# Kernel tuning notes

Hardware: AMD Instinct MI355X
Metric: run time of the kernel (lower is better)

## Reference

```python
import jax, jax.numpy as jnp
import numpy as np

KSIZE = 3
KN = (KSIZE - 1) // 2  # 1
TEMP = 50.0


def _extract_patches(x, same_pad):
    """TF tf.image.extract_patches ordering: per location, (dy, dx, channel).
    x: [b,H,W,d] -> [b,h,w,9*d] (h=H,w=W if same_pad else H-2,W-2)."""
    if same_pad:
        x = jnp.pad(x, ((0, 0), (KN, KN), (KN, KN), (0, 0)))
    b, Hp, Wp, d = x.shape
    h, w = Hp - 2 * KN, Wp - 2 * KN
    slices = [x[:, dy:dy + h, dx:dx + w, :]
              for dy in range(KSIZE) for dx in range(KSIZE)]
    return jnp.concatenate(slices, axis=-1)


def setup_inputs() -> dict:
    key = jax.random.key(0)
    k1, k2, k3 = jax.random.split(key, 3)
    b, h, w, dims = 4, 48, 48, 64
    g_in = jax.random.normal(k1, (b, h, w, dims), dtype=jnp.float32)
    # binary inpainting mask (1 = known background, 0 = hole)
    mask = (jax.random.uniform(k2, (b, h, w, 1)) > 0.5).astype(jnp.float32)
    W2 = jax.random.normal(k3, (2 * dims, dims), dtype=jnp.float32) / np.sqrt(2.0 * dims)
    b2 = jnp.zeros((dims,), dtype=jnp.float32)
    return {"g_in": g_in, "mask": mask, "W2": W2, "b2": b2}


def reference(g_in, mask, W2, b2):
    b, h, w, dims = g_in.shape
    c = (h - 2 * KN) * (w - 2 * KN)

    mask_r = mask  # already (h,w,1); broadcasts over dims (== tile)
    bg = g_in * mask_r

    # p1: VALID 3x3 patches of bg -> dynamic kernels, [b, c, 9*dims]
    p1 = _extract_patches(bg, same_pad=False).reshape(b, c, KSIZE * KSIZE * dims)
    # p2: SAME 3x3 patches of g_in, [b, h, w, 9*dims]
    p2 = _extract_patches(g_in, same_pad=True)

    # cross-correlation: conv2d(ft, k1) == per-location dot with each bg patch
    CS = jnp.einsum('byxk,bjk->byxj', p2, p1)              # [b,h,w,c]
    k1d = jnp.sum(p1 * p1, axis=2)                          # [b,c]
    wwd = jnp.sum(p2 * p2, axis=3, keepdims=True)           # [b,h,w,1]
    DS1 = k1d[:, None, None, :] + wwd - 2.0 * CS            # squared distances
    mu = jnp.mean(DS1, axis=3, keepdims=True)
    sd = jnp.std(DS1, axis=3, keepdims=True)                # population std (tf.math.reduce_std)
    DS2 = -jnp.tanh((DS1 - mu) / sd)
    CA = jax.nn.softmax(TEMP * DS2, axis=-1)                # [b,h,w,c]

    # transposed conv aggregation with per-sample kernels k2[b,j,dy,dx,ch]
    k2 = p1.reshape(b, c, KSIZE, KSIZE, dims)
    CA_pad = jnp.pad(CA, ((0, 0), (KN, KN), (KN, KN), (0, 0)))
    acl = jnp.zeros((b, h, w, dims), dtype=g_in.dtype)
    for dy in range(KSIZE):
        for dx in range(KSIZE):
            win = CA_pad[:, 2 * KN - dy:2 * KN - dy + h, 2 * KN - dx:2 * KN - dx + w, :]
            acl = acl + jnp.einsum('byxj,bjd->byxd', win, k2[:, :, dy, dx, :])
    acl = acl / 9.0

    ACL = bg + acl * (1.0 - mask_r)
    con1 = jnp.concatenate([g_in, ACL], axis=3)             # [b,h,w,2*dims]
    return jax.nn.elu(jnp.einsum('byxk,kd->byxd', con1, W2) + b2)
```

## Files before the change

kernel.cpp:

```cpp
#include <hip/hip_runtime.h>
#include <hip/hip_fp16.h>
#include <math.h>

#define BB 4
#define HH 48
#define WW 48
#define DD 64
#define CH 46
#define CWp 46
#define CC (CH*CWp)
#define KK 576
#define HWp (HH*WW)
#define KPAD 2176
#define KSPLIT0 1088
#define PW 50
#define PP (PW*PW)

typedef __attribute__((ext_vector_type(8))) short short8;
typedef __attribute__((ext_vector_type(4))) float float4v;

#define OFFB_GPAD  ((size_t)0)
#define OFFB_BGPAD ((size_t)1280000)
#define OFFB_E     ((size_t)2560000)
#define OFFB_K1D   ((size_t)2596864)
#define OFFB_P1T   ((size_t)2630720)
#define OFFB_S     ((size_t)12657728)
#define OFFB_AGG0  ((size_t)52765760)
#define OFFB_AGG1  ((size_t)63382592)

__device__ __forceinline__ ushort f2bf(float x) {
    unsigned u = __float_as_uint(x);
    return (ushort)((u + 0x7FFFu + ((u >> 16) & 1u)) >> 16);
}

__device__ __forceinline__ float waveReduceSum(float x) {
#pragma unroll
    for (int o = 32; o > 0; o >>= 1) x += __shfl_down(x, o, 64);
    return x;
}

__device__ __forceinline__ float blockReduceSum(float x, float* sm) {
#pragma unroll
    for (int o = 32; o > 0; o >>= 1) x += __shfl_down(x, o, 64);
    int lane = threadIdx.x & 63, w = threadIdx.x >> 6;
    __syncthreads();
    if (lane == 0) sm[w] = x;
    __syncthreads();
    return sm[0] + sm[1] + sm[2] + sm[3];
}

__device__ __forceinline__ float fast_tanh(float z) {
    float e = __expf(2.f * z);
    return 1.f - 2.f / (e + 1.f);
}

typedef __attribute__((address_space(3))) void lds_void_t;
typedef __attribute__((address_space(1))) void gmem_void_t;
__device__ __forceinline__ void gld16(const ushort* g, ushort* lds) {
    __builtin_amdgcn_global_load_lds((gmem_void_t*)g, (lds_void_t*)lds, 16, 0, 0);
}

__global__ __launch_bounds__(256) void build_pads(const float* __restrict__ g,
                                                  const float* __restrict__ mask,
                                                  ushort* __restrict__ gpad,
                                                  ushort* __restrict__ bgpad,
                                                  float* __restrict__ e) {
    int w = threadIdx.x >> 6, c = threadIdx.x & 63;
    int q4 = blockIdx.x * 4 + w;
    int b = q4 / PP, q = q4 % PP;
    int yp = q / PW, xp = q % PW;
    size_t o = (size_t)q4 * DD + c;
    if (yp >= 1 && yp <= HH && xp >= 1 && xp <= WW) {
        int pix = (yp - 1) * WW + (xp - 1);
        float gv = g[((size_t)b * HWp + pix) * DD + c];
        float m  = mask[(size_t)b * HWp + pix];
        float bgv = gv * m;
        gpad[o]  = f2bf(gv);
        bgpad[o] = f2bf(bgv);
        float ss = waveReduceSum(bgv * bgv);
        if (c == 0) e[b * HWp + pix] = ss;
    } else {
        gpad[o] = 0;
        bgpad[o] = 0;
    }
}

__global__ __launch_bounds__(256) void build_p1t(const ushort* __restrict__ bgpad,
                                                 const float* __restrict__ e,
                                                 ushort* __restrict__ p1t,
                                                 float* __restrict__ k1d) {
    int d9 = blockIdx.y, b = blockIdx.z;
    int t = threadIdx.x;
    if (blockIdx.x == 34) {
        int jg = (b * 9 + d9) * 256 + t;
        if (jg < BB * CC) {
            int bb = jg / CC, j = jg % CC;
            int jy = j / CWp, jx = j - jy * CWp;
            const float* eb = e + bb * HWp + jy * WW + jx;
            float s = 0.f;
#pragma unroll
            for (int ddy = 0; ddy < 3; ddy++)
#pragma unroll
                for (int ddx = 0; ddx < 3; ddx++) s += eb[ddy * WW + ddx];
            k1d[jg] = s;
        }
        return;
    }
    __shared__ ushort T[64 * 65];
    int jt = blockIdx.x;
    int dy = d9 / 3, dx = d9 - dy * 3;
    const ushort* src = bgpad + (size_t)b * PP * DD;
    int lr = t >> 3, c8 = (t & 7) * 8;
#pragma unroll
    for (int pass = 0; pass < 2; pass++) {
        int r = lr + pass * 32;
        int j = jt * 64 + r;
        uint4 d = make_uint4(0, 0, 0, 0);
        if (j < CC) {
            int jy = j / CWp, jx = j - jy * CWp;
            d = *(const uint4*)(src + (size_t)((jy + dy + 1) * PW + (jx + dx + 1)) * DD + c8);
        }
        ushort tmp[8];
        *(uint4*)tmp = d;
#pragma unroll
        for (int u = 0; u < 8; u++) T[r * 65 + c8 + u] = tmp[u];
    }
    __syncthreads();
#pragma unroll
    for (int pass = 0; pass < 2; pass++) {
        int c = lr + pass * 32;
        int j8 = (t & 7) * 8;
        ushort tmp[8];
#pragma unroll
        for (int u = 0; u < 8; u++) tmp[u] = T[(j8 + u) * 65 + c];
        *(uint4*)(p1t + ((size_t)b * KK + d9 * 64 + c) * KPAD + jt * 64 + j8) = *(const uint4*)tmp;
    }
}

__global__ __launch_bounds__(256) void gemm1_nt(const ushort* __restrict__ gpad,
                                                const ushort* __restrict__ bgpad,
                                                __half* __restrict__ Cout) {
    __shared__ ushort As[2 * 4096];
    __shared__ ushort Bs[2 * 4096];
    int i0 = blockIdx.x;
    int b = (i0 & 7) >> 1;
    int tile = ((i0 >> 3) << 1) | (i0 & 1);
    int ty = tile / 17, tx = tile - ty * 17;
    int m0 = ty * 128, n0 = tx * 128;
    const ushort* Ag = gpad + (size_t)b * PP * DD;
    const ushort* Bg = bgpad + (size_t)b * PP * DD;

    int tid = threadIdx.x;
    int l = tid & 63, w = tid >> 6;
    int quad = l >> 4, l15 = l & 15;
    int sw8 = (l15 >> 1) & 3;
    int wm = (w >> 1) * 64, wn = (w & 1) * 64;
    int rowInC = l >> 2;
    int cSw = (l & 3) ^ ((l >> 3) & 3);

    int baseA[2], baseB[2];
    bool vB[2];
#pragma unroll
    for (int i = 0; i < 2; i++) {
        int rg = w * 2 + i;
        int r = rg * 16 + rowInC;
        int p = m0 + r;
        int y = p / WW, x = p - y * WW;
        baseA[i] = (y * PW + x) * DD + cSw * 8;
        int n = n0 + r;
        vB[i] = (n < CC);
        int jy = 0, jx = 0;
        if (vB[i]) { jy = n / CWp; jx = n - jy * CWp; }
        baseB[i] = ((jy + 1) * PW + (jx + 1)) * DD + cSw * 8;
    }

    float4v acc[4][4];
#pragma unroll
    for (int i = 0; i < 4; i++)
#pragma unroll
        for (int j = 0; j < 4; j++) acc[i][j] = (float4v){0.f, 0.f, 0.f, 0.f};

#pragma unroll
    for (int i = 0; i < 2; i++) {
        int rg = w * 2 + i;
        gld16(Ag + baseA[i], As + rg * 512);
        if (vB[i]) gld16(Bg + baseB[i], Bs + rg * 512);
    }

    int buf = 0;
    for (int k0 = 0; k0 < KK; k0 += 32) {
        __syncthreads();
        int nb = buf ^ 1;
        int kn = k0 + 32;
        if (kn < KK) {
            int d9 = kn >> 6;
            int dy = d9 / 3, dx = d9 - dy * 3;
            int off = (dy * PW + dx) * DD + (kn & 63);
#pragma unroll
            for (int i = 0; i < 2; i++) {
                int rg = w * 2 + i;
                gld16(Ag + baseA[i] + off, As + nb * 4096 + rg * 512);
                if (vB[i]) gld16(Bg + baseB[i] + off, Bs + nb * 4096 + rg * 512);
            }
        }
        const ushort* Ax = As + buf * 4096;
        const ushort* Bx = Bs + buf * 4096;
        short8 af[4], bf[4];
#pragma unroll
        for (int i = 0; i < 4; i++)
            af[i] = *(const short8*)&Ax[(wm + i * 16 + l15) * 32 + ((quad ^ sw8)) * 8];
#pragma unroll
        for (int j = 0; j < 4; j++)
            bf[j] = *(const short8*)&Bx[(wn + j * 16 + l15) * 32 + ((quad ^ sw8)) * 8];
#pragma unroll
        for (int i = 0; i < 4; i++)
#pragma unroll
            for (int j = 0; j < 4; j++)
                acc[i][j] = __builtin_amdgcn_mfma_f32_16x16x32_bf16(af[i], bf[j], acc[i][j], 0, 0, 0);
        buf = nb;
    }

    __half* C = Cout + (size_t)b * HWp * KPAD;
#pragma unroll
    for (int i = 0; i < 4; i++) {
#pragma unroll
        for (int j = 0; j < 4; j++) {
            int n = n0 + wn + j * 16 + l15;
            if (n < CC) {
#pragma unroll
                for (int r = 0; r < 4; r++) {
                    int m = m0 + wm + i * 16 + quad * 4 + r;
                    C[(size_t)m * KPAD + n] = __float2half(acc[i][j][r]);
                }
            }
        }
    }
}

template <int NF, bool NMASK>
__device__ __forceinline__ void gemm_tile_db(const ushort* __restrict__ Ab,
                                             const ushort* __restrict__ Bb,
                                             int lda, int ldb, int kb, int ke,
                                             int Nrem,
                                             ushort* As, ushort* Bs,
                                             float4v (&acc)[4][NF]) {
    constexpr int NBI = NF / 2;
    constexpr int BBUF = 2048 * NBI;
    int tid = threadIdx.x;
    int l = tid & 63, w = tid >> 6;
    int quad = l >> 4, l15 = l & 15;
    int sw8 = (l15 >> 1) & 3;
    int wm = (w >> 1) * 64, wn = (w & 1) * (NF * 16);
    int rowInC = l >> 2;
    int cSw = (l & 3) ^ ((l >> 3) & 3);

#pragma unroll
    for (int i = 0; i < 2; i++) {
        int rg = w * 2 + i;
        gld16(Ab + (size_t)(rg * 16 + rowInC) * lda + kb + cSw * 8, As + rg * 512);
    }
#pragma unroll
    for (int i = 0; i < NBI; i++) {
        int rg = w * NBI + i;
        int r = rg * 16 + rowInC;
        if (!NMASK || r < Nrem)
            gld16(Bb + (size_t)r * ldb + kb + cSw * 8, Bs + rg * 512);
    }

    int buf = 0;
    for (int k0 = kb; k0 < ke; k0 += 32) {
        __syncthreads();
        int nb = buf ^ 1;
        if (k0 + 32 < ke) {
#pragma unroll
            for (int i = 0; i < 2; i++) {
                int rg = w * 2 + i;
                gld16(Ab + (size_t)(rg * 16 + rowInC) * lda + (k0 + 32) + cSw * 8,
                      As + nb * 4096 + rg * 512);
            }
#pragma unroll
            for (int i = 0; i < NBI; i++) {
                int rg = w * NBI + i;
                int r = rg * 16 + rowInC;
                if (!NMASK || r < Nrem)
                    gld16(Bb + (size_t)r * ldb + (k0 + 32) + cSw * 8,
                          Bs + nb * BBUF + rg * 512);
            }
        }
        const ushort* Ax = As + buf * 4096;
        const ushort* Bx = Bs + buf * BBUF;
        short8 af[4], bf[NF];
#pragma unroll
        for (int i = 0; i < 4; i++)
            af[i] = *(const short8*)&Ax[(wm + i * 16 + l15) * 32 + ((quad ^ sw8)) * 8];
#pragma unroll
        for (int j = 0; j < NF; j++)
            bf[j] = *(const short8*)&Bx[(wn + j * 16 + l15) * 32 + ((quad ^ sw8)) * 8];
#pragma unroll
        for (int i = 0; i < 4; i++)
#pragma unroll
            for (int j = 0; j < NF; j++)
                acc[i][j] = __builtin_amdgcn_mfma_f32_16x16x32_bf16(af[i], bf[j], acc[i][j], 0, 0, 0);
        buf = nb;
    }
}

__global__ __launch_bounds__(256) void gemm2_split(const ushort* __restrict__ A,
                                                   const ushort* __restrict__ Bt,
                                                   __half* __restrict__ agg0,
                                                   __half* __restrict__ agg1) {
    __shared__ ushort As[2 * 4096];
    __shared__ ushort Bs[2 * 6144];
    int i0 = blockIdx.x;
    int z = i0 & 7;
    int b = z >> 1, split = z & 1;
    int tile = i0 >> 3;
    int ty = tile / 3, tx = tile - ty * 3;
    int m0 = ty * 128, n0 = tx * 192;
    const ushort* Ab = A + (size_t)b * HWp * KPAD + (size_t)m0 * KPAD;
    const ushort* Bb = Bt + (size_t)b * KK * KPAD + (size_t)n0 * KPAD;
    float4v acc[4][6];
#pragma unroll
    for (int i = 0; i < 4; i++)
#pragma unroll
        for (int j = 0; j < 6; j++) acc[i][j] = (float4v){0.f, 0.f, 0.f, 0.f};

    gemm_tile_db<6, false>(Ab, Bb, KPAD, KPAD, split ? KSPLIT0 : 0,
                           split ? KPAD : KSPLIT0, 192, As, Bs, acc);

    int tid = threadIdx.x;
    int lane = tid & 63, wid = tid >> 6;
    int quad = lane >> 4, l15 = lane & 15;
    int wm = (wid >> 1) * 64, wn = (wid & 1) * 96;
    __half* C = (split ? agg1 : agg0) + (size_t)b * HWp * KK;
#pragma unroll
    for (int i = 0; i < 4; i++) {
#pragma unroll
        for (int j = 0; j < 6; j++) {
            int n = n0 + wn + j * 16 + l15;
#pragma unroll
            for (int r = 0; r < 4; r++) {
                int m = m0 + wm + i * 16 + quad * 4 + r;
                C[(size_t)m * KK + n] = __float2half(acc[i][j][r]);
            }
        }
    }
}

__global__ __launch_bounds__(256) void rowsoft(void* __restrict__ Sbase,
                                               const float* __restrict__ k1d) {
    __shared__ float sm[4];
    size_t row = blockIdx.x;
    int b = (int)(row / HWp);
    const __half* p = (const __half*)Sbase + row * KPAD;
    ushort* wout = (ushort*)Sbase + row * KPAD;
    const float* k1 = k1d + (size_t)b * CC;
    int t = threadIdx.x;
    bool hasx = t < 34;

    uint4 raw = *(const uint4*)(p + t * 8);
    uint rx = hasx ? *(const uint*)(p + 2048 + t * 2) : 0u;
    float v[8], vx[2];
    {
        const __half2* h2 = (const __half2*)&raw;
#pragma unroll
        for (int i = 0; i < 4; i++) {
            float2 f = __half22float2(h2[i]);
            v[2 * i] = f.x; v[2 * i + 1] = f.y;
        }
        __half2 hx = *(__half2*)&rx;
        float2 fx = __half22float2(hx);
        vx[0] = fx.x; vx[1] = fx.y;
    }
    {
        const float* kp = k1 + t * 8;
#pragma unroll
        for (int i = 0; i < 8; i++) v[i] = kp[i] - 2.f * v[i];
        if (hasx) {
            vx[0] = k1[2048 + t * 2] - 2.f * vx[0];
            vx[1] = k1[2048 + t * 2 + 1] - 2.f * vx[1];
        }
    }
    float s = 0.f;
#pragma unroll
    for (int i = 0; i < 8; i++) s += v[i];
    if (hasx) s += vx[0] + vx[1];
    s = blockReduceSum(s, sm);
    float mu = s / (float)CC;
    float vs = 0.f;
#pragma unroll
    for (int i = 0; i < 8; i++) { float d = v[i] - mu; vs += d * d; }
    if (hasx) { float d0 = vx[0] - mu, d1 = vx[1] - mu; vs += d0 * d0 + d1 * d1; }
    vs = blockReduceSum(vs, sm);
    float inv_sd = 1.f / sqrtf(vs / (float)CC);
    float es = 0.f;
#pragma unroll
    for (int i = 0; i < 8; i++) {
        v[i] = __expf(-50.f * fast_tanh((v[i] - mu) * inv_sd));
        es += v[i];
    }
    if (hasx) {
        vx[0] = __expf(-50.f * fast_tanh((vx[0] - mu) * inv_sd));
        vx[1] = __expf(-50.f * fast_tanh((vx[1] - mu) * inv_sd));
        es += vx[0] + vx[1];
    }
    es = blockReduceSum(es, sm);
    float invz = 1.f / es;

    ushort o[8];
#pragma unroll
    for (int i = 0; i < 8; i++) o[i] = f2bf(v[i] * invz);
    *(uint4*)(wout + t * 8) = *(const uint4*)o;
    if (hasx) {
        ushort ox[2] = { f2bf(vx[0] * invz), f2bf(vx[1] * invz) };
        *(uint*)(wout + 2048 + t * 2) = *(const uint*)ox;
    } else {
        *(uint*)(wout + CC + 2 * (t - 34)) = 0u;
    }
}

__global__ __launch_bounds__(256) void final_k(const float* __restrict__ g,
                                               const float* __restrict__ mask,
                                               const __half* __restrict__ agg0,
                                               const __half* __restrict__ agg1,
                                               const float* __restrict__ W2,
                                               const float* __restrict__ b2,
                                               float* __restrict__ out) {
    int w = threadIdx.x >> 6, d = threadIdx.x & 63;
    int pix = blockIdx.x * 4 + w;
    int b = pix / HWp, yx = pix % HWp;
    int y = yx / WW, x = yx % WW;

    __shared__ float con1[4][128];
    float acl = 0.f;
#pragma unroll
    for (int dy = 0; dy < 3; dy++) {
#pragma unroll
        for (int dx = 0; dx < 3; dx++) {
            int yy = y + 1 - dy, xx = x + 1 - dx;
            if (yy >= 0 && yy < HH && xx >= 0 && xx < WW) {
                size_t off = ((size_t)(b * HWp + yy * WW + xx)) * KK + (dy * 3 + dx) * DD + d;
                acl += __half2float(agg0[off]) + __half2float(agg1[off]);
            }
        }
    }
    float m = mask[pix];
    float gv = g[(size_t)pix * DD + d];
    float bgv = gv * m;
    float ACL = bgv + (acl / 9.f) * (1.f - m);
    con1[w][d] = gv;
    con1[w][64 + d] = ACL;
    __syncthreads();
    float accv = b2[d];
#pragma unroll 8
    for (int k = 0; k < 128; k++) accv = fmaf(con1[w][k], W2[k * 64 + d], accv);
    out[(size_t)pix * DD + d] = accv > 0.f ? accv : expm1f(accv);
}

extern "C" void kernel_launch(void* const* d_in, const int* in_sizes, int n_in,
                              void* d_out, int out_size, void* d_ws, size_t ws_size,
                              hipStream_t stream) {
    const float* g    = (const float*)d_in[0];
    const float* mask = (const float*)d_in[1];
    const float* W2   = (const float*)d_in[2];
    const float* b2   = (const float*)d_in[3];
    float* out = (float*)d_out;
    char* ws = (char*)d_ws;

    ushort* gpad  = (ushort*)(ws + OFFB_GPAD);
    ushort* bgpad = (ushort*)(ws + OFFB_BGPAD);
    float*  e     = (float*) (ws + OFFB_E);
    float*  k1d   = (float*) (ws + OFFB_K1D);
    ushort* p1t   = (ushort*)(ws + OFFB_P1T);
    void*   S     = (void*)  (ws + OFFB_S);
    __half* agg0  = (__half*)(ws + OFFB_AGG0);
    __half* agg1  = (__half*)(ws + OFFB_AGG1);

    build_pads<<<BB * PP / 4, 256, 0, stream>>>(g, mask, gpad, bgpad, e);
    build_p1t<<<dim3(35, 9, BB), 256, 0, stream>>>(bgpad, e, p1t, k1d);

    gemm1_nt<<<dim3(1224), 256, 0, stream>>>(gpad, bgpad, (__half*)S);

    rowsoft<<<BB * HWp, 256, 0, stream>>>(S, k1d);

    gemm2_split<<<dim3(432), 256, 0, stream>>>((const ushort*)S, p1t, agg0, agg1);

    final_k<<<BB * HWp / 4, 256, 0, stream>>>(g, mask, agg0, agg1, W2, b2, out);
}
```

Before: 187.9 us.

## Factor patch correlation into pixel-level Gram matrix plus 3x3 stencil sums

```diff
diff --git a/kernel.cpp b/kernel.cpp
--- a/kernel.cpp
+++ b/kernel.cpp
@@ -7,14 +7,15 @@
 #define WW 48
 #define DD 64
 #define CH 46
-#define CWp 46
-#define CC (CH*CWp)
-#define KK 576
+#define CC (CH*CH)
 #define HWp (HH*WW)
-#define KPAD 2176
-#define KSPLIT0 1088
 #define PW 50
 #define PP (PW*PW)
+#define UST 2512
+#define CAST 2120
+#define QN 2304
+#define NSPL 8
+#define KCH (QN/NSPL)
 
 typedef __attribute__((ext_vector_type(8))) short short8;
 typedef __attribute__((ext_vector_type(4))) float float4v;
@@ -23,14 +24,18 @@
 #define OFFB_BGPAD ((size_t)1280000)
 #define OFFB_E     ((size_t)2560000)
 #define OFFB_K1D   ((size_t)2596864)
-#define OFFB_P1T   ((size_t)2630720)
-#define OFFB_S     ((size_t)12657728)
-#define OFFB_AGG0  ((size_t)52765760)
-#define OFFB_AGG1  ((size_t)63382592)
+#define OFFB_BGT   ((size_t)2630720)
+#define OFFB_U     ((size_t)3810368)
+#define OFFB_CA    ((size_t)54050368)
+#define OFFB_WGT   ((size_t)93126208)
+#define OFFB_ACLP  ((size_t)135593536)
 
 __device__ __forceinline__ ushort f2bf(float x) {
     unsigned u = __float_as_uint(x);
     return (ushort)((u + 0x7FFFu + ((u >> 16) & 1u)) >> 16);
+}
+__device__ __forceinline__ float bf2f(ushort h) {
+    return __uint_as_float((unsigned)h << 16);
 }
 
 __device__ __forceinline__ float waveReduceSum(float x) {
@@ -85,94 +90,83 @@
     }
 }
 
-__global__ __launch_bounds__(256) void build_p1t(const ushort* __restrict__ bgpad,
-                                                 const float* __restrict__ e,
-                                                 ushort* __restrict__ p1t,
-                                                 float* __restrict__ k1d) {
-    int d9 = blockIdx.y, b = blockIdx.z;
+__global__ __launch_bounds__(256) void build_bgt_k1d(const ushort* __restrict__ bgpad,
+                                                     const float* __restrict__ e,
+                                                     ushort* __restrict__ bgT,
+                                                     float* __restrict__ k1d) {
     int t = threadIdx.x;
-    if (blockIdx.x == 34) {
-        int jg = (b * 9 + d9) * 256 + t;
+    if (blockIdx.x < 144) {
+        int b = blockIdx.x / 36, tile = blockIdx.x % 36;
+        __shared__ ushort T[64 * 65];
+        const ushort* src = bgpad + (size_t)b * PP * DD;
+        int lr = t >> 3, c8 = (t & 7) * 8;
+#pragma unroll
+        for (int pass = 0; pass < 2; pass++) {
+            int r = lr + pass * 32;
+            int p = tile * 64 + r;
+            int py = p / 48 + 1, px = p % 48 + 1;
+            uint4 d = *(const uint4*)(src + (size_t)(py * PW + px) * DD + c8);
+            ushort tmp[8];
+            *(uint4*)tmp = d;
+#pragma unroll
+            for (int u = 0; u < 8; u++) T[r * 65 + c8 + u] = tmp[u];
+        }
+        __syncthreads();
+        ushort* dst = bgT + (size_t)b * DD * QN;
+#pragma unroll
+        for (int pass = 0; pass < 2; pass++) {
+            int c = lr + pass * 32;
+            int j8 = (t & 7) * 8;
+            ushort tmp[8];
+#pragma unroll
+            for (int u = 0; u < 8; u++) tmp[u] = T[(j8 + u) * 65 + c];
+            *(uint4*)(dst + (size_t)c * QN + tile * 64 + j8) = *(const uint4*)tmp;
+        }
+    } else {
+        int jg = (blockIdx.x - 144) * 256 + t;
         if (jg < BB * CC) {
-            int bb = jg / CC, j = jg % CC;
-            int jy = j / CWp, jx = j - jy * CWp;
-            const float* eb = e + bb * HWp + jy * WW + jx;
+            int b = jg / CC, j = jg % CC;
+            int jy = j / CH, jx = j - jy * CH;
+            const float* eb = e + b * HWp + jy * WW + jx;
             float s = 0.f;
 #pragma unroll
-            for (int ddy = 0; ddy < 3; ddy++)
-#pragma unroll
-                for (int ddx = 0; ddx < 3; ddx++) s += eb[ddy * WW + ddx];
+            for (int dy = 0; dy < 3; dy++)
+#pragma unroll
+                for (int dx = 0; dx < 3; dx++) s += eb[dy * WW + dx];
             k1d[jg] = s;
         }
-        return;
-    }
-    __shared__ ushort T[64 * 65];
-    int jt = blockIdx.x;
-    int dy = d9 / 3, dx = d9 - dy * 3;
-    const ushort* src = bgpad + (size_t)b * PP * DD;
-    int lr = t >> 3, c8 = (t & 7) * 8;
-#pragma unroll
-    for (int pass = 0; pass < 2; pass++) {
-        int r = lr + pass * 32;
-        int j = jt * 64 + r;
-        uint4 d = make_uint4(0, 0, 0, 0);
-        if (j < CC) {
-            int jy = j / CWp, jx = j - jy * CWp;
-            d = *(const uint4*)(src + (size_t)((jy + dy + 1) * PW + (jx + dx + 1)) * DD + c8);
-        }
-        ushort tmp[8];
-        *(uint4*)tmp = d;
-#pragma unroll
-        for (int u = 0; u < 8; u++) T[r * 65 + c8 + u] = tmp[u];
-    }
-    __syncthreads();
-#pragma unroll
-    for (int pass = 0; pass < 2; pass++) {
-        int c = lr + pass * 32;
-        int j8 = (t & 7) * 8;
-        ushort tmp[8];
-#pragma unroll
-        for (int u = 0; u < 8; u++) tmp[u] = T[(j8 + u) * 65 + c];
-        *(uint4*)(p1t + ((size_t)b * KK + d9 * 64 + c) * KPAD + jt * 64 + j8) = *(const uint4*)tmp;
-    }
-}
-
-__global__ __launch_bounds__(256) void gemm1_nt(const ushort* __restrict__ gpad,
-                                                const ushort* __restrict__ bgpad,
-                                                __half* __restrict__ Cout) {
-    __shared__ ushort As[2 * 4096];
-    __shared__ ushort Bs[2 * 4096];
+    }
+}
+
+__global__ __launch_bounds__(256) void ugemm(const ushort* __restrict__ gpad,
+                                             const ushort* __restrict__ bgpad,
+                                             __half* __restrict__ U) {
+    __shared__ ushort As[128 * 64];
+    __shared__ ushort Bs[128 * 64];
     int i0 = blockIdx.x;
     int b = (i0 & 7) >> 1;
     int tile = ((i0 >> 3) << 1) | (i0 & 1);
-    int ty = tile / 17, tx = tile - ty * 17;
-    int m0 = ty * 128, n0 = tx * 128;
+    int ty = tile / 20, tx = tile - ty * 20;
+    int p0 = ty * 128, q0 = tx * 128;
     const ushort* Ag = gpad + (size_t)b * PP * DD;
     const ushort* Bg = bgpad + (size_t)b * PP * DD;
 
     int tid = threadIdx.x;
     int l = tid & 63, w = tid >> 6;
     int quad = l >> 4, l15 = l & 15;
-    int sw8 = (l15 >> 1) & 3;
+    int sw = l15 & 7;
     int wm = (w >> 1) * 64, wn = (w & 1) * 64;
-    int rowInC = l >> 2;
-    int cSw = (l & 3) ^ ((l >> 3) & 3);
-
-    int baseA[2], baseB[2];
-    bool vB[2];
-#pragma unroll
-    for (int i = 0; i < 2; i++) {
-        int rg = w * 2 + i;
-        int r = rg * 16 + rowInC;
-        int p = m0 + r;
-        int y = p / WW, x = p - y * WW;
-        baseA[i] = (y * PW + x) * DD + cSw * 8;
-        int n = n0 + r;
-        vB[i] = (n < CC);
-        int jy = 0, jx = 0;
-        if (vB[i]) { jy = n / CWp; jx = n - jy * CWp; }
-        baseB[i] = ((jy + 1) * PW + (jx + 1)) * DD + cSw * 8;
-    }
+    int sr = l >> 3;
+    int gch = (l & 7) ^ (sr & 7);
+
+#pragma unroll
+    for (int i = 0; i < 4; i++) {
+        int rg = 4 * w + i;
+        int r = rg * 8 + sr;
+        if (p0 + r < PP) gld16(Ag + (size_t)(p0 + r) * DD + gch * 8, As + rg * 512);
+        if (q0 + r < PP) gld16(Bg + (size_t)(q0 + r) * DD + gch * 8, Bs + rg * 512);
+    }
+    __syncthreads();
 
     float4v acc[4][4];
 #pragma unroll
@@ -181,59 +175,137 @@
         for (int j = 0; j < 4; j++) acc[i][j] = (float4v){0.f, 0.f, 0.f, 0.f};
 
 #pragma unroll
-    for (int i = 0; i < 2; i++) {
-        int rg = w * 2 + i;
-        gld16(Ag + baseA[i], As + rg * 512);
-        if (vB[i]) gld16(Bg + baseB[i], Bs + rg * 512);
-    }
-
-    int buf = 0;
-    for (int k0 = 0; k0 < KK; k0 += 32) {
-        __syncthreads();
-        int nb = buf ^ 1;
-        int kn = k0 + 32;
-        if (kn < KK) {
-            int d9 = kn >> 6;
-            int dy = d9 / 3, dx = d9 - dy * 3;
-            int off = (dy * PW + dx) * DD + (kn & 63);
-#pragma unroll
-            for (int i = 0; i < 2; i++) {
-                int rg = w * 2 + i;
-                gld16(Ag + baseA[i] + off, As + nb * 4096 + rg * 512);
-                if (vB[i]) gld16(Bg + baseB[i] + off, Bs + nb * 4096 + rg * 512);
-            }
-        }
-        const ushort* Ax = As + buf * 4096;
-        const ushort* Bx = Bs + buf * 4096;
+    for (int h = 0; h < 2; h++) {
         short8 af[4], bf[4];
 #pragma unroll
         for (int i = 0; i < 4; i++)
-            af[i] = *(const short8*)&Ax[(wm + i * 16 + l15) * 32 + ((quad ^ sw8)) * 8];
+            af[i] = *(const short8*)&As[(wm + i * 16 + l15) * 64 + ((h * 4 + quad) ^ sw) * 8];
 #pragma unroll
         for (int j = 0; j < 4; j++)
-            bf[j] = *(const short8*)&Bx[(wn + j * 16 + l15) * 32 + ((quad ^ sw8)) * 8];
+            bf[j] = *(const short8*)&Bs[(wn + j * 16 + l15) * 64 + ((h * 4 + quad) ^ sw) * 8];
 #pragma unroll
         for (int i = 0; i < 4; i++)
 #pragma unroll
             for (int j = 0; j < 4; j++)
                 acc[i][j] = __builtin_amdgcn_mfma_f32_16x16x32_bf16(af[i], bf[j], acc[i][j], 0, 0, 0);
-        buf = nb;
-    }
-
-    __half* C = Cout + (size_t)b * HWp * KPAD;
+    }
+
+    __half* Ub = U + (size_t)b * PP * UST;
 #pragma unroll
     for (int i = 0; i < 4; i++) {
 #pragma unroll
         for (int j = 0; j < 4; j++) {
-            int n = n0 + wn + j * 16 + l15;
-            if (n < CC) {
+            int n = q0 + wn + j * 16 + l15;
+            if (n < PP) {
 #pragma unroll
                 for (int r = 0; r < 4; r++) {
-                    int m = m0 + wm + i * 16 + quad * 4 + r;
-                    C[(size_t)m * KPAD + n] = __float2half(acc[i][j][r]);
+                    int m = p0 + wm + i * 16 + quad * 4 + r;
+                    if (m < PP) Ub[(size_t)m * UST + n] = __float2half(acc[i][j][r]);
                 }
             }
         }
+    }
+}
+
+__global__ __launch_bounds__(256) void cs_softmax(const __half* __restrict__ U,
+                                                  const float* __restrict__ k1d,
+                                                  ushort* __restrict__ CA) {
+    __shared__ float sm[4];
+    int i0 = blockIdx.x;
+    int b = (i0 & 7) >> 1;
+    int m = ((i0 >> 3) << 1) | (i0 & 1);
+    int y = m / 48, x = m - y * 48;
+    const __half* Ub = U + (size_t)b * PP * UST;
+    const float* k1 = k1d + b * CC;
+    const __half* rows[9];
+#pragma unroll
+    for (int dy = 0; dy < 3; dy++)
+#pragma unroll
+        for (int dx = 0; dx < 3; dx++)
+            rows[dy * 3 + dx] = Ub + (size_t)((y + dy) * PW + (x + dx)) * UST;
+
+    int t = threadIdx.x;
+    float v[9];
+#pragma unroll
+    for (int i = 0; i < 9; i++) {
+        int j = t + i * 256;
+        if (j < CC) {
+            int jy = j / CH, jx = j - jy * CH;
+            int base = (jy + 1) * PW + (jx + 1);
+            float cs = 0.f;
+#pragma unroll
+            for (int s = 0; s < 9; s++) {
+                int off = (s / 3) * PW + (s % 3);
+                cs += __half2float(rows[s][base + off]);
+            }
+            v[i] = k1[j] - 2.f * cs;
+        } else v[i] = 0.f;
+    }
+    float s0 = 0.f;
+#pragma unroll
+    for (int i = 0; i < 9; i++) { int j = t + i * 256; if (j < CC) s0 += v[i]; }
+    s0 = blockReduceSum(s0, sm);
+    float mu = s0 / (float)CC;
+    float vs = 0.f;
+#pragma unroll
+    for (int i = 0; i < 9; i++) {
+        int j = t + i * 256;
+        if (j < CC) { float d = v[i] - mu; vs += d * d; }
+    }
+    vs = blockReduceSum(vs, sm);
+    float inv_sd = 1.f / sqrtf(vs / (float)CC);
+    float es = 0.f;
+#pragma unroll
+    for (int i = 0; i < 9; i++) {
+        int j = t + i * 256;
+        if (j < CC) {
+            v[i] = __expf(-50.f * fast_tanh((v[i] - mu) * inv_sd));
+            es += v[i];
+        }
+    }
+    es = blockReduceSum(es, sm);
+    float invz = 1.f / es;
+    ushort* wout = CA + (size_t)(b * HWp + m) * CAST;
+#pragma unroll
+    for (int i = 0; i < 9; i++) {
+        int j = t + i * 256;
+        if (j < CAST) wout[j] = (j < CC) ? f2bf(v[i] * invz) : (ushort)0;
+    }
+}
+
+__global__ __launch_bounds__(256) void wgt_gather(const ushort* __restrict__ CA,
+                                                  ushort* __restrict__ Wgt) {
+    int i0 = blockIdx.x;
+    int b = (i0 & 7) >> 1;
+    int m = ((i0 >> 3) << 1) | (i0 & 1);
+    int y = m / 48, x = m - y * 48;
+    const ushort* CAb = CA + (size_t)b * HWp * CAST;
+    const ushort* rows[9];
+    bool val[9];
+#pragma unroll
+    for (int dy = 0; dy < 3; dy++)
+#pragma unroll
+        for (int dx = 0; dx < 3; dx++) {
+            int my = y + 1 - dy, mx = x + 1 - dx;
+            bool ok = ((unsigned)my < 48u) && ((unsigned)mx < 48u);
+            val[dy * 3 + dx] = ok;
+            rows[dy * 3 + dx] = CAb + (size_t)(ok ? (my * 48 + mx) : 0) * CAST;
+        }
+    ushort* out = Wgt + (size_t)(b * HWp + m) * QN;
+    int t = threadIdx.x;
+#pragma unroll
+    for (int i = 0; i < 9; i++) {
+        int q = t + i * 256;
+        int qy = q / 48, qx = q - qy * 48;
+        float ws = 0.f;
+#pragma unroll
+        for (int s = 0; s < 9; s++) {
+            int dy = s / 3, dx = s % 3;
+            int jy = qy - dy, jx = qx - dx;
+            if (val[s] && (unsigned)jy < (unsigned)CH && (unsigned)jx < (unsigned)CH)
+                ws += bf2f(rows[s][jy * CH + jx]);
+        }
+        out[q] = f2bf(ws);
     }
 }
 
@@ -244,7 +316,7 @@
                                              int Nrem,
                                              ushort* As, ushort* Bs,
                                              float4v (&acc)[4][NF]) {
-    constexpr int NBI = NF / 2;
+    constexpr int NBI = (NF + 1) / 2;
     constexpr int BBUF = 2048 * NBI;
     int tid = threadIdx.x;
     int l = tid & 63, w = tid >> 6;
@@ -305,149 +377,65 @@
     }
 }
 
-__global__ __launch_bounds__(256) void gemm2_split(const ushort* __restrict__ A,
-                                                   const ushort* __restrict__ Bt,
-                                                   __half* __restrict__ agg0,
-                                                   __half* __restrict__ agg1) {
+__global__ __launch_bounds__(256) void acl_gemm(const ushort* __restrict__ Wgt,
+                                                const ushort* __restrict__ bgT,
+                                                __half* __restrict__ aclP) {
     __shared__ ushort As[2 * 4096];
-    __shared__ ushort Bs[2 * 6144];
+    __shared__ ushort Bs[2 * 2048];
     int i0 = blockIdx.x;
-    int z = i0 & 7;
-    int b = z >> 1, split = z & 1;
-    int tile = i0 >> 3;
-    int ty = tile / 3, tx = tile - ty * 3;
-    int m0 = ty * 128, n0 = tx * 192;
-    const ushort* Ab = A + (size_t)b * HWp * KPAD + (size_t)m0 * KPAD;
-    const ushort* Bb = Bt + (size_t)b * KK * KPAD + (size_t)n0 * KPAD;
-    float4v acc[4][6];
+    int z = i0 & 31;
+    int b = z >> 3, split = z & 7;
+    int ty = i0 >> 5;
+    int m0 = ty * 128;
+    const ushort* Ab = Wgt + (size_t)b * HWp * QN + (size_t)m0 * QN;
+    const ushort* Bb = bgT + (size_t)b * DD * QN;
+    float4v acc[4][2];
 #pragma unroll
     for (int i = 0; i < 4; i++)
 #pragma unroll
-        for (int j = 0; j < 6; j++) acc[i][j] = (float4v){0.f, 0.f, 0.f, 0.f};
-
-    gemm_tile_db<6, false>(Ab, Bb, KPAD, KPAD, split ? KSPLIT0 : 0,
-                           split ? KPAD : KSPLIT0, 192, As, Bs, acc);
+        for (int j = 0; j < 2; j++) acc[i][j] = (float4v){0.f, 0.f, 0.f, 0.f};
+
+    int kb = split * KCH;
+    gemm_tile_db<2, false>(Ab, Bb, QN, QN, kb, kb + KCH, DD, As, Bs, acc);
 
     int tid = threadIdx.x;
     int lane = tid & 63, wid = tid >> 6;
     int quad = lane >> 4, l15 = lane & 15;
-    int wm = (wid >> 1) * 64, wn = (wid & 1) * 96;
-    __half* C = (split ? agg1 : agg0) + (size_t)b * HWp * KK;
+    int wm = (wid >> 1) * 64, wn = (wid & 1) * 32;
+    __half* C = aclP + (size_t)(split * BB + b) * HWp * DD;
 #pragma unroll
     for (int i = 0; i < 4; i++) {
 #pragma unroll
-        for (int j = 0; j < 6; j++) {
-            int n = n0 + wn + j * 16 + l15;
+        for (int j = 0; j < 2; j++) {
+            int n = wn + j * 16 + l15;
 #pragma unroll
             for (int r = 0; r < 4; r++) {
                 int m = m0 + wm + i * 16 + quad * 4 + r;
-                C[(size_t)m * KK + n] = __float2half(acc[i][j][r]);
+                C[(size_t)m * DD + n] = __float2half(acc[i][j][r]);
             }
         }
-    }
-}
-
-__global__ __launch_bounds__(256) void rowsoft(void* __restrict__ Sbase,
-                                               const float* __restrict__ k1d) {
-    __shared__ float sm[4];
-    size_t row = blockIdx.x;
-    int b = (int)(row / HWp);
-    const __half* p = (const __half*)Sbase + row * KPAD;
-    ushort* wout = (ushort*)Sbase + row * KPAD;
-    const float* k1 = k1d + (size_t)b * CC;
-    int t = threadIdx.x;
-    bool hasx = t < 34;
-
-    uint4 raw = *(const uint4*)(p + t * 8);
-    uint rx = hasx ? *(const uint*)(p + 2048 + t * 2) : 0u;
-    float v[8], vx[2];
-    {
-        const __half2* h2 = (const __half2*)&raw;
-#pragma unroll
-        for (int i = 0; i < 4; i++) {
-            float2 f = __half22float2(h2[i]);
-            v[2 * i] = f.x; v[2 * i + 1] = f.y;
-        }
-        __half2 hx = *(__half2*)&rx;
-        float2 fx = __half22float2(hx);
-        vx[0] = fx.x; vx[1] = fx.y;
-    }
-    {
-        const float* kp = k1 + t * 8;
-#pragma unroll
-        for (int i = 0; i < 8; i++) v[i] = kp[i] - 2.f * v[i];
-        if (hasx) {
-            vx[0] = k1[2048 + t * 2] - 2.f * vx[0];
-            vx[1] = k1[2048 + t * 2 + 1] - 2.f * vx[1];
-        }
-    }
-    float s = 0.f;
-#pragma unroll
-    for (int i = 0; i < 8; i++) s += v[i];
-    if (hasx) s += vx[0] + vx[1];
-    s = blockReduceSum(s, sm);
-    float mu = s / (float)CC;
-    float vs = 0.f;
-#pragma unroll
-    for (int i = 0; i < 8; i++) { float d = v[i] - mu; vs += d * d; }
-    if (hasx) { float d0 = vx[0] - mu, d1 = vx[1] - mu; vs += d0 * d0 + d1 * d1; }
-    vs = blockReduceSum(vs, sm);
-    float inv_sd = 1.f / sqrtf(vs / (float)CC);
-    float es = 0.f;
-#pragma unroll
-    for (int i = 0; i < 8; i++) {
-        v[i] = __expf(-50.f * fast_tanh((v[i] - mu) * inv_sd));
-        es += v[i];
-    }
-    if (hasx) {
-        vx[0] = __expf(-50.f * fast_tanh((vx[0] - mu) * inv_sd));
-        vx[1] = __expf(-50.f * fast_tanh((vx[1] - mu) * inv_sd));
-        es += vx[0] + vx[1];
-    }
-    es = blockReduceSum(es, sm);
-    float invz = 1.f / es;
-
-    ushort o[8];
-#pragma unroll
-    for (int i = 0; i < 8; i++) o[i] = f2bf(v[i] * invz);
-    *(uint4*)(wout + t * 8) = *(const uint4*)o;
-    if (hasx) {
-        ushort ox[2] = { f2bf(vx[0] * invz), f2bf(vx[1] * invz) };
-        *(uint*)(wout + 2048 + t * 2) = *(const uint*)ox;
-    } else {
-        *(uint*)(wout + CC + 2 * (t - 34)) = 0u;
     }
 }
 
 __global__ __launch_bounds__(256) void final_k(const float* __restrict__ g,
                                                const float* __restrict__ mask,
-                                               const __half* __restrict__ agg0,
-                                               const __half* __restrict__ agg1,
+                                               const __half* __restrict__ aclP,
                                                const float* __restrict__ W2,
                                                const float* __restrict__ b2,
                                                float* __restrict__ out) {
     int w = threadIdx.x >> 6, d = threadIdx.x & 63;
     int pix = blockIdx.x * 4 + w;
-    int b = pix / HWp, yx = pix % HWp;
-    int y = yx / WW, x = yx % WW;
+    int b = pix / HWp, m = pix % HWp;
 
     __shared__ float con1[4][128];
     float acl = 0.f;
 #pragma unroll
-    for (int dy = 0; dy < 3; dy++) {
-#pragma unroll
-        for (int dx = 0; dx < 3; dx++) {
-            int yy = y + 1 - dy, xx = x + 1 - dx;
-            if (yy >= 0 && yy < HH && xx >= 0 && xx < WW) {
-                size_t off = ((size_t)(b * HWp + yy * WW + xx)) * KK + (dy * 3 + dx) * DD + d;
-                acl += __half2float(agg0[off]) + __half2float(agg1[off]);
-            }
-        }
-    }
-    float m = mask[pix];
+    for (int s = 0; s < NSPL; s++)
+        acl += __half2float(aclP[((size_t)(s * BB + b) * HWp + m) * DD + d]);
+    float mk = mask[pix];
     float gv = g[(size_t)pix * DD + d];
-    float bgv = gv * m;
-    float ACL = bgv + (acl / 9.f) * (1.f - m);
+    float bgv = gv * mk;
+    float ACL = bgv + (acl / 9.f) * (1.f - mk);
     con1[w][d] = gv;
     con1[w][64 + d] = ACL;
     __syncthreads();
@@ -471,19 +459,22 @@
     ushort* bgpad = (ushort*)(ws + OFFB_BGPAD);
     float*  e     = (float*) (ws + OFFB_E);
     float*  k1d   = (float*) (ws + OFFB_K1D);
-    ushort* p1t   = (ushort*)(ws + OFFB_P1T);
-    void*   S     = (void*)  (ws + OFFB_S);
-    __half* agg0  = (__half*)(ws + OFFB_AGG0);
-    __half* agg1  = (__half*)(ws + OFFB_AGG1);
+    ushort* bgT   = (ushort*)(ws + OFFB_BGT);
+    __half* U     = (__half*)(ws + OFFB_U);
+    ushort* CA    = (ushort*)(ws + OFFB_CA);
+    ushort* Wgt   = (ushort*)(ws + OFFB_WGT);
+    __half* aclP  = (__half*)(ws + OFFB_ACLP);
 
     build_pads<<<BB * PP / 4, 256, 0, stream>>>(g, mask, gpad, bgpad, e);
-    build_p1t<<<dim3(35, 9, BB), 256, 0, stream>>>(bgpad, e, p1t, k1d);
-
-    gemm1_nt<<<dim3(1224), 256, 0, stream>>>(gpad, bgpad, (__half*)S);
-
-    rowsoft<<<BB * HWp, 256, 0, stream>>>(S, k1d);
-
-    gemm2_split<<<dim3(432), 256, 0, stream>>>((const ushort*)S, p1t, agg0, agg1);
-
-    final_k<<<BB * HWp / 4, 256, 0, stream>>>(g, mask, agg0, agg1, W2, b2, out);
-}
+    build_bgt_k1d<<<144 + 34, 256, 0, stream>>>(bgpad, e, bgT, k1d);
+
+    ugemm<<<dim3(1600), 256, 0, stream>>>(gpad, bgpad, U);
+
+    cs_softmax<<<dim3(8 * 1152), 256, 0, stream>>>(U, k1d, CA);
+
+    wgt_gather<<<dim3(8 * 1152), 256, 0, stream>>>(CA, Wgt);
+
+    acl_gemm<<<dim3(576), 256, 0, stream>>>(Wgt, bgT, aclP);
+
+    final_k<<<BB * HWp / 4, 256, 0, stream>>>(g, mask, aclP, W2, b2, out);
+}
```

Measured after the change: 270.0 us. 1.44x slower.

## Load gemm1 MFMA fragments directly from global into registers, bypassing LDS

Applied to the files above, without the earlier changes.

```diff
diff --git a/kernel.cpp b/kernel.cpp
--- a/kernel.cpp
+++ b/kernel.cpp
@@ -140,8 +140,6 @@
 __global__ __launch_bounds__(256) void gemm1_nt(const ushort* __restrict__ gpad,
                                                 const ushort* __restrict__ bgpad,
                                                 __half* __restrict__ Cout) {
-    __shared__ ushort As[2 * 4096];
-    __shared__ ushort Bs[2 * 4096];
     int i0 = blockIdx.x;
     int b = (i0 & 7) >> 1;
     int tile = ((i0 >> 3) << 1) | (i0 & 1);
@@ -153,25 +151,21 @@
     int tid = threadIdx.x;
     int l = tid & 63, w = tid >> 6;
     int quad = l >> 4, l15 = l & 15;
-    int sw8 = (l15 >> 1) & 3;
     int wm = (w >> 1) * 64, wn = (w & 1) * 64;
-    int rowInC = l >> 2;
-    int cSw = (l & 3) ^ ((l >> 3) & 3);
-
-    int baseA[2], baseB[2];
-    bool vB[2];
-#pragma unroll
-    for (int i = 0; i < 2; i++) {
-        int rg = w * 2 + i;
-        int r = rg * 16 + rowInC;
-        int p = m0 + r;
+
+    const ushort* Arow[4];
+    const ushort* Brow[4];
+    bool vN[4];
+#pragma unroll
+    for (int i = 0; i < 4; i++) {
+        int p = m0 + wm + i * 16 + l15;
         int y = p / WW, x = p - y * WW;
-        baseA[i] = (y * PW + x) * DD + cSw * 8;
-        int n = n0 + r;
-        vB[i] = (n < CC);
+        Arow[i] = Ag + (size_t)(y * PW + x) * DD + quad * 8;
+        int n = n0 + wn + i * 16 + l15;
+        vN[i] = (n < CC);
         int jy = 0, jx = 0;
-        if (vB[i]) { jy = n / CWp; jx = n - jy * CWp; }
-        baseB[i] = ((jy + 1) * PW + (jx + 1)) * DD + cSw * 8;
+        if (vN[i]) { jy = n / CWp; jx = n - jy * CWp; }
+        Brow[i] = Bg + (size_t)((jy + 1) * PW + (jx + 1)) * DD + quad * 8;
     }
 
     float4v acc[4][4];
@@ -180,44 +174,31 @@
 #pragma unroll
         for (int j = 0; j < 4; j++) acc[i][j] = (float4v){0.f, 0.f, 0.f, 0.f};
 
-#pragma unroll
-    for (int i = 0; i < 2; i++) {
-        int rg = w * 2 + i;
-        gld16(Ag + baseA[i], As + rg * 512);
-        if (vB[i]) gld16(Bg + baseB[i], Bs + rg * 512);
-    }
-
-    int buf = 0;
-    for (int k0 = 0; k0 < KK; k0 += 32) {
-        __syncthreads();
-        int nb = buf ^ 1;
-        int kn = k0 + 32;
-        if (kn < KK) {
-            int d9 = kn >> 6;
-            int dy = d9 / 3, dx = d9 - dy * 3;
-            int off = (dy * PW + dx) * DD + (kn & 63);
-#pragma unroll
-            for (int i = 0; i < 2; i++) {
-                int rg = w * 2 + i;
-                gld16(Ag + baseA[i] + off, As + nb * 4096 + rg * 512);
-                if (vB[i]) gld16(Bg + baseB[i] + off, Bs + nb * 4096 + rg * 512);
-            }
-        }
-        const ushort* Ax = As + buf * 4096;
-        const ushort* Bx = Bs + buf * 4096;
-        short8 af[4], bf[4];
+    short8 af[2][4], bf[2][4];
+#pragma unroll
+    for (int i = 0; i < 4; i++) {
+        af[0][i] = *(const short8*)(Arow[i]);
+        bf[0][i] = *(const short8*)(Brow[i]);
+    }
+
+#pragma unroll
+    for (int it = 0; it < 18; it++) {
+        const int cur = it & 1, nxt = cur ^ 1;
+        if (it + 1 < 18) {
+            const int kn = (it + 1) * 32;
+            const int d9 = kn >> 6;
+            const int off = ((d9 / 3) * PW + (d9 % 3)) * DD + (kn & 63);
+#pragma unroll
+            for (int i = 0; i < 4; i++) {
+                af[nxt][i] = *(const short8*)(Arow[i] + off);
+                bf[nxt][i] = *(const short8*)(Brow[i] + off);
+            }
+        }
 #pragma unroll
         for (int i = 0; i < 4; i++)
-            af[i] = *(const short8*)&Ax[(wm + i * 16 + l15) * 32 + ((quad ^ sw8)) * 8];
-#pragma unroll
-        for (int j = 0; j < 4; j++)
-            bf[j] = *(const short8*)&Bx[(wn + j * 16 + l15) * 32 + ((quad ^ sw8)) * 8];
-#pragma unroll
-        for (int i = 0; i < 4; i++)
 #pragma unroll
             for (int j = 0; j < 4; j++)
-                acc[i][j] = __builtin_amdgcn_mfma_f32_16x16x32_bf16(af[i], bf[j], acc[i][j], 0, 0, 0);
-        buf = nb;
+                acc[i][j] = __builtin_amdgcn_mfma_f32_16x16x32_bf16(af[cur][i], bf[cur][j], acc[i][j], 0, 0, 0);
     }
 
     __half* C = Cout + (size_t)b * HWp * KPAD;
```

After: 249.7 us. +32.9%, slower.
